# Optimization experiments

Measured on AMD Instinct MI355X. Metric: run time of the kernel, lower is better.

Reference implementation:

```python
import jax, jax.numpy as jnp
import numpy as np
from jax import lax

N = 100000      # nodes
E = 1600000     # edges
T = 8           # timesteps
DS, DT = 10, 20 # static / temporal features
GH = 64         # gnn_hidden
LH = 64         # lstm_hidden
EC = 64         # end_channels
OC = 1          # out_channels
EPS = 1e-5


def setup_inputs() -> dict:
    key = jax.random.key(0)
    ks = jax.random.split(key, 20)
    g = lambda i, shape, s=0.05: jax.random.normal(ks[i], shape, jnp.float32) * s
    return {
        "x": jax.random.normal(ks[0], (N, DS + DT, T), jnp.float32),
        "edge_index": jax.random.randint(ks[1], (2, E), 0, N, jnp.int64),
        # static encoder (computed in forward but unused downstream, kept for faithfulness)
        "W_static": g(2, (GH, DS)), "b_static": g(3, (GH,)),
        # LSTMCell: input_size = DT + GH, hidden = LH; gate order i,f,g,o
        "W_ih": g(4, (4 * LH, DT + GH)), "W_hh": g(5, (4 * LH, LH)),
        "b_ih": g(6, (4 * LH,)), "b_hh": g(7, (4 * LH,)),
        # GraphConv(lstm_hidden -> gnn_hidden): lin_rel (with bias) on aggregated msgs + lin_root (no bias)
        "W_rel": g(8, (GH, LH)), "b_rel": g(9, (GH,)), "W_root": g(10, (GH, LH)),
        # BatchNorm1d(GH+LH)
        "gamma": jnp.ones((GH + LH,), jnp.float32), "beta": jnp.zeros((GH + LH,), jnp.float32),
        # head: linear1(128->EC), linear2(EC->128), output_layer(128->OC)
        "W1": g(11, (EC, GH + LH)), "b1": g(12, (EC,)),
        "W2": g(13, (GH + LH, EC)), "b2": g(14, (GH + LH,)),
        "W_out": g(15, (OC, GH + LH)), "b_out": g(16, (OC,)),
    }


def reference(x, edge_index, W_static, b_static, W_ih, W_hh, b_ih, b_hh,
              W_rel, b_rel, W_root, gamma, beta, W1, b1, W2, b2, W_out, b_out):
    src, dst = edge_index[0], edge_index[1]
    x_static = x[:, :DS, 0]                      # [N, DS]
    x_temporal = x[:, DS:DS + DT, :]             # [N, DT, T]
    static_embed = x_static @ W_static.T + b_static  # computed but unused (matches source)

    xt_seq = jnp.transpose(x_temporal, (2, 0, 1))  # [T, N, DT]
    h0 = jnp.zeros((N, GH), jnp.float32)
    c0 = jnp.zeros((N, GH), jnp.float32)

    def step(carry, x_t):
        h, c = carry
        # GraphConv: sum-aggregate neighbor h, then linear (linear commutes with sum)
        agg = jax.ops.segment_sum(h[src], dst, num_segments=N)   # [N, LH]
        gnn_out = agg @ W_rel.T + b_rel + h @ W_root.T           # [N, GH]
        inp = jnp.concatenate([x_t, gnn_out], axis=1)            # [N, DT+GH]
        gates = inp @ W_ih.T + b_ih + h @ W_hh.T + b_hh          # [N, 4*LH]
        i, f, g_, o = jnp.split(gates, 4, axis=1)
        c_new = jax.nn.sigmoid(f) * c + jax.nn.sigmoid(i) * jnp.tanh(g_)
        h_new = jax.nn.sigmoid(o) * jnp.tanh(c_new)
        return (h_new, c_new), gnn_out

    (h, c), gnn_outs = lax.scan(step, (h0, c0), xt_seq)
    gnn_out = gnn_outs[-1]  # gnn output computed at the last timestep (pre-update h)

    fused = jnp.concatenate([h, gnn_out], axis=1)                # [N, GH+LH]
    # BatchNorm1d, training-mode batch statistics (dropout p set to 0)
    mean = fused.mean(axis=0)
    var = fused.var(axis=0)
    normed = (fused - mean) * lax.rsqrt(var + EPS) * gamma + beta
    h1 = jax.nn.relu(normed @ W1.T + b1)
    hidden = jax.nn.relu(h1 @ W2.T + b2)
    out = jax.nn.sigmoid(hidden @ W_out.T + b_out)               # binary task -> sigmoid
    return out
```

## Files before the change

kernel.cpp:

```cpp
#include <hip/hip_runtime.h>

#define NN 100000
#define NE 1600000
#define TT 8
#define KF 160
#define XSTR 24
#define HISTB 6250
#define NRANGE 8
#define RSPAN 12500

typedef __attribute__((ext_vector_type(8))) short bf16x8;
typedef __attribute__((ext_vector_type(4))) float f32x4;
typedef unsigned int uint_;
typedef unsigned short ushort_;
typedef __attribute__((ext_vector_type(4))) uint_ u32x4;

__device__ __forceinline__ float sigf(float x) { return 1.f / (1.f + __expf(-x)); }
__device__ __forceinline__ float tanhf_(float x) { return 1.f - 2.f / (__expf(2.f * x) + 1.f); }
__device__ __forceinline__ ushort_ f2b(float f) {
    uint_ u = __float_as_uint(f);
    u += 0x7fff + ((u >> 16) & 1);
    return (ushort_)(u >> 16);
}
__device__ __forceinline__ float bl(uint_ u) { return __uint_as_float(u << 16); }
__device__ __forceinline__ float bh(uint_ u) { return __uint_as_float(u & 0xffff0000u); }
__device__ __forceinline__ void acc8(float* a, uint4 v) {
    a[0] += bl(v.x); a[1] += bh(v.x); a[2] += bl(v.y); a[3] += bh(v.y);
    a[4] += bl(v.z); a[5] += bh(v.z); a[6] += bl(v.w); a[7] += bh(v.w);
}
__device__ __forceinline__ uint_ pk(float a, float b) {
    return (uint_)f2b(a) | ((uint_)f2b(b) << 16);
}
__device__ __forceinline__ uint4 ntld16(const void* p) {
    u32x4 v = __builtin_nontemporal_load((const u32x4*)p);
    return make_uint4(v[0], v[1], v[2], v[3]);
}

__global__ void k_detect(const int* __restrict__ ei, int* flag) {
    int i = blockIdx.x * 256 + threadIdx.x;
    if (ei[2 * i + 1] != 0) atomicOr(flag, 1);
}

__global__ void k_hist_xt(const int* __restrict__ ei, const int* __restrict__ flag, int* cnt,
                          const float* __restrict__ x, ushort_* __restrict__ xT) {
    int b = blockIdx.x;
    if (b < HISTB) {
        int e = b * 256 + threadIdx.x;
        if (e >= NE) return;
        int is32 = *flag;
        int d = is32 ? ei[NE + e] : ei[2 * (NE + e)];
        atomicAdd(&cnt[d], 1);
    } else {
        if (!xT) return;
        int i = (b - HISTB) * 256 + threadIdx.x;
        if (i >= NN * XSTR) return;
        int n = i / XSTR, kk = i - n * XSTR;
        if (kk < 20) {
            const float* xp = x + (size_t)n * 240 + (10 + kk) * 8;
#pragma unroll
            for (int t = 0; t < 8; t++) xT[(size_t)t * NN * XSTR + i] = f2b(xp[t]);
        } else {
#pragma unroll
            for (int t = 0; t < 8; t++) xT[(size_t)t * NN * XSTR + i] = 0;
        }
    }
}

__global__ void k_scanblk(const int* __restrict__ cnt, int* off, int* bsum) {
    __shared__ int tmp[1024];
    int i = blockIdx.x * 1024 + threadIdx.x;
    int v = (i < NN) ? cnt[i] : 0;
    tmp[threadIdx.x] = v;
    __syncthreads();
    for (int d = 1; d < 1024; d <<= 1) {
        int t = (threadIdx.x >= d) ? tmp[threadIdx.x - d] : 0;
        __syncthreads();
        tmp[threadIdx.x] += t;
        __syncthreads();
    }
    if (i < NN) off[i + 1] = tmp[threadIdx.x];
    if (threadIdx.x == 1023) bsum[blockIdx.x] = tmp[1023];
}

__global__ void k_scantop(int* bsum, int nb) {
    if (threadIdx.x == 0) {
        int run = 0;
        for (int b = 0; b < nb; b++) { int t = bsum[b]; bsum[b] = run; run += t; }
    }
}

__global__ void k_scanadd(int* off, const int* __restrict__ bsum) {
    int i = blockIdx.x * 1024 + threadIdx.x;
    if (i < NN) off[i + 1] += bsum[blockIdx.x];
    if (i == 0) off[0] = 0;
}

__global__ void k_scatter(const int* __restrict__ ei, const int* __restrict__ flag,
                          int* cursor, int* csr) {
    int b = blockIdx.x;
    int range = b & (NRANGE - 1), chunk = b >> 3;
    int e = chunk * 256 + threadIdx.x;
    if (e >= NE) return;
    int is32 = *flag;
    int d = is32 ? ei[NE + e] : ei[2 * (NE + e)];
    if (d / RSPAN != range) return;
    int s = is32 ? ei[e] : ei[2 * e];
    int pos = atomicAdd(&cursor[d], 1);
    csr[pos] = s;
}

__global__ void k_prep(const float* __restrict__ W_ih, const float* __restrict__ W_hh,
                       const float* __restrict__ b_ih, const float* __restrict__ b_hh,
                       const float* __restrict__ W_rel, const float* __restrict__ b_rel,
                       const float* __restrict__ W_root, ushort_* WgB, float* bgp) {
    int n = threadIdx.x;
    int k = blockIdx.x;
    if (k < KF) {
        float v = 0.f;
        if (n < 256) {
            int w = n >> 6, g = (n >> 4) & 3, j = w * 16 + (n & 15);
            int row = g * 64 + j;
            if (k < 20) {
                v = W_ih[row * 84 + k];
            } else if (k >= 24 && k < 88) {
                int kk = k - 24;
                float a = 0.f;
                for (int m = 0; m < 64; m++) a += W_ih[row * 84 + 20 + m] * W_rel[m * 64 + kk];
                v = a;
            } else if (k >= 88 && k < 152) {
                int kk = k - 88;
                float a = W_hh[row * 64 + kk];
                for (int m = 0; m < 64; m++) a += W_ih[row * 84 + 20 + m] * W_root[m * 64 + kk];
                v = a;
            }
        } else {
            int j = n - 256;
            if (k >= 24 && k < 88) v = W_rel[j * 64 + (k - 24)];
            else if (k >= 88 && k < 152) v = W_root[j * 64 + (k - 88)];
        }
        WgB[(size_t)n * KF + k] = f2b(v);
    } else {
        if (n < 256) {
            int j = n >> 2, g = n & 3;
            int row = g * 64 + j;
            float a = b_ih[row] + b_hh[row];
            for (int m = 0; m < 64; m++) a += W_ih[row * 84 + 20 + m] * b_rel[m];
            bgp[n] = a;
        } else {
            bgp[n] = b_rel[n - 256];
        }
    }
}

template <bool LAST>
__device__ __forceinline__ void step_body(const float* __restrict__ x,
                                          const ushort_* __restrict__ xT,
                                          const int* __restrict__ off,
                                          const int* __restrict__ csr,
                                          const ushort_* __restrict__ hbR,
                                          ushort_* __restrict__ hbW,
                                          float* __restrict__ hf,
                                          float* __restrict__ c,
                                          const ushort_* __restrict__ WgB,
                                          const float* __restrict__ bgp,
                                          float* __restrict__ gnn,
                                          float* __restrict__ sums,
                                          float* __restrict__ sumsq, int t) {
    __shared__ __align__(16) ushort_ Zs[64 * 168];
    const int tid = threadIdx.x;
    const int nblk = blockIdx.x * 64;
    const int w = tid >> 6, lane = tid & 63;
    const int q = lane >> 4, l16 = lane & 15;

#pragma unroll
    for (int i = 0; i < 3; ++i) {
        int slot = tid + 256 * i;
        int n = slot / 12, oo = slot - n * 12;
        int n_g = nblk + n;
        uint4 z = make_uint4(0, 0, 0, 0);
        if (n_g < NN) {
            if (oo < 3) {
                if (xT) {
                    z = ntld16(xT + ((size_t)t * NN + n_g) * XSTR + oo * 8);
                } else {
                    const float* xp = x + (size_t)n_g * 240 + 80 + (size_t)oo * 64 + t;
                    uint_ r[4];
#pragma unroll
                    for (int p = 0; p < 4; p++) {
                        int k0 = oo * 8 + p * 2;
                        ushort_ b0 = (k0 < 20) ? f2b(xp[p * 16]) : (ushort_)0;
                        ushort_ b1 = (k0 + 1 < 20) ? f2b(xp[p * 16 + 8]) : (ushort_)0;
                        r[p] = (uint_)b0 | ((uint_)b1 << 16);
                    }
                    z = make_uint4(r[0], r[1], r[2], r[3]);
                }
            } else if (oo < 11) {
                if (t > 0)
                    z = *(const uint4*)(hbR + (size_t)n_g * 64 + (oo - 3) * 8);
            }
        }
        int oct = (oo < 3) ? oo : ((oo < 11) ? (oo + 8) : 19);
        *(uint4*)(Zs + n * 168 + oct * 8) = z;
    }

    {
        int slot = tid >> 3;
        int l8 = tid & 7;
        for (int nn = slot; nn < 64; nn += 32) {
            int node = nblk + nn;
            float a[8];
#pragma unroll
            for (int i = 0; i < 8; i++) a[i] = 0.f;
            if (t > 0 && node < NN) {
                int e0 = off[node], e1 = off[node + 1];
                int e = e0;
                if (e + 8 <= e1) {
                    uint4 v[8];
#pragma unroll
                    for (int i = 0; i < 8; i++)
                        v[i] = *(const uint4*)(hbR + (size_t)csr[e + i] * 64 + l8 * 8);
                    e += 8;
                    for (; e + 8 <= e1; e += 8) {
#pragma unroll
                        for (int i = 0; i < 4; i++) {
                            acc8(a, v[i]);
                            v[i] = *(const uint4*)(hbR + (size_t)csr[e + i] * 64 + l8 * 8);
                        }
#pragma unroll
                        for (int i = 4; i < 8; i++) {
                            acc8(a, v[i]);
                            v[i] = *(const uint4*)(hbR + (size_t)csr[e + i] * 64 + l8 * 8);
                        }
                    }
#pragma unroll
                    for (int i = 0; i < 8; i++) acc8(a, v[i]);
                }
                for (; e < e1; e++) {
                    uint4 v0 = *(const uint4*)(hbR + (size_t)csr[e] * 64 + l8 * 8);
                    acc8(a, v0);
                }
            }
            uint4 o;
            o.x = pk(a[0], a[1]); o.y = pk(a[2], a[3]);
            o.z = pk(a[4], a[5]); o.w = pk(a[6], a[7]);
            *(uint4*)(Zs + nn * 168 + 24 + l8 * 8) = o;
        }
    }
    __syncthreads();

    const int j = w * 16 + l16;
    float sh = 0.f, sh2 = 0.f, sg = 0.f, sg2 = 0.f;

    if (LAST) {
        f32x4 accg[4];
#pragma unroll
        for (int mt = 0; mt < 4; mt++) accg[mt] = (f32x4)(0.f);
#pragma unroll
        for (int kt = 0; kt < 5; ++kt) {
            bf16x8 bfg = *(const bf16x8*)(WgB + (size_t)(256 + w * 16 + l16) * KF + kt * 32 + q * 8);
#pragma unroll
            for (int mt = 0; mt < 4; mt++) {
                bf16x8 af = *(const bf16x8*)(Zs + (mt * 16 + l16) * 168 + kt * 32 + q * 8);
                accg[mt] = __builtin_amdgcn_mfma_f32_16x16x32_bf16(af, bfg, accg[mt], 0, 0, 0);
            }
        }
        const float brl = bgp[256 + j];
#pragma unroll
        for (int mt = 0; mt < 4; ++mt)
#pragma unroll
            for (int r = 0; r < 4; ++r) {
                int node = nblk + mt * 16 + q * 4 + r;
                if (node < NN) {
                    float gn = accg[mt][r] + brl;
                    gnn[(size_t)node * 64 + j] = gn;
                    sg += gn; sg2 += gn * gn;
                }
            }
    }

    f32x4 acc[4][4];
#pragma unroll
    for (int mt = 0; mt < 4; mt++)
#pragma unroll
        for (int nt = 0; nt < 4; nt++) acc[mt][nt] = (f32x4)(0.f);

#pragma unroll
    for (int kt = 0; kt < 5; ++kt) {
        bf16x8 af[4], bf[4];
#pragma unroll
        for (int mt = 0; mt < 4; mt++)
            af[mt] = *(const bf16x8*)(Zs + (mt * 16 + l16) * 168 + kt * 32 + q * 8);
#pragma unroll
        for (int nt = 0; nt < 4; nt++) {
            int n = w * 64 + nt * 16 + l16;
            bf[nt] = *(const bf16x8*)(WgB + (size_t)n * KF + kt * 32 + q * 8);
        }
#pragma unroll
        for (int mt = 0; mt < 4; mt++)
#pragma unroll
            for (int nt = 0; nt < 4; nt++)
                acc[mt][nt] = __builtin_amdgcn_mfma_f32_16x16x32_bf16(af[mt], bf[nt], acc[mt][nt], 0, 0, 0);
    }

    const f32x4 bias = *(const f32x4*)(bgp + j * 4);

    __syncthreads();
    ushort_* Hs   = Zs;
    float*   CsLo = (float*)(Zs + 4096);

    float cnHi[8];
#pragma unroll
    for (int mt = 0; mt < 4; ++mt) {
#pragma unroll
        for (int r = 0; r < 4; ++r) {
            int nloc = mt * 16 + q * 4 + r;
            int node = nblk + nloc;
            float cn = 0.f, hn = 0.f;
            if (node < NN) {
                size_t idx = (size_t)node * 64 + j;
                float iv = sigf(acc[mt][0][r] + bias.x);
                float fv = sigf(acc[mt][1][r] + bias.y);
                float gv = tanhf_(acc[mt][2][r] + bias.z);
                float ov = sigf(acc[mt][3][r] + bias.w);
                float cold = 0.f;
                if (t > 0) cold = __builtin_nontemporal_load(c + idx);
                cn = fv * cold + iv * gv;
                hn = ov * tanhf_(cn);
                if (LAST) {
                    hf[idx] = hn;
                    sh += hn; sh2 += hn * hn;
                }
            }
            Hs[nloc * 64 + j] = f2b(hn);
            if (mt < 2) CsLo[nloc * 64 + j] = cn;
            else        cnHi[(mt - 2) * 4 + r] = cn;
        }
    }
    __syncthreads();
#pragma unroll
    for (int i = 0; i < 2; ++i) {
        int s = tid + 256 * i;
        {
            int n = s >> 3, part = s & 7;
            if (nblk + n < NN)
                *(uint4*)(hbW + (size_t)(nblk + n) * 64 + part * 8) =
                    *(const uint4*)(Hs + n * 64 + part * 8);
        }
        {
            int n = s >> 4, part = s & 15;
            if (nblk + n < NN)
                *(float4*)(c + (size_t)(nblk + n) * 64 + part * 4) =
                    *(const float4*)(CsLo + n * 64 + part * 4);
        }
    }
    __syncthreads();
    float* CsHi = (float*)Zs;
#pragma unroll
    for (int mt = 2; mt < 4; ++mt)
#pragma unroll
        for (int r = 0; r < 4; ++r) {
            int nloc = mt * 16 + q * 4 + r;
            CsHi[(nloc - 32) * 64 + j] = cnHi[(mt - 2) * 4 + r];
        }
    __syncthreads();
#pragma unroll
    for (int i = 0; i < 2; ++i) {
        int s = tid + 256 * i;
        int n = 32 + (s >> 4), part = s & 15;
        if (nblk + n < NN)
            *(float4*)(c + (size_t)(nblk + n) * 64 + part * 4) =
                *(const float4*)(CsHi + (n - 32) * 64 + part * 4);
    }

    if (LAST) {
#pragma unroll
        for (int d = 16; d < 64; d <<= 1) {
            sh += __shfl_xor(sh, d, 64);
            sh2 += __shfl_xor(sh2, d, 64);
            sg += __shfl_xor(sg, d, 64);
            sg2 += __shfl_xor(sg2, d, 64);
        }
        if (q == 0) {
            atomicAdd(&sums[j], sh);
            atomicAdd(&sumsq[j], sh2);
            atomicAdd(&sums[64 + j], sg);
            atomicAdd(&sumsq[64 + j], sg2);
        }
    }
}

__global__ __launch_bounds__(256, 4) void k_step(const float* __restrict__ x,
                                                 const ushort_* __restrict__ xT,
                                                 const int* __restrict__ off,
                                                 const int* __restrict__ csr,
                                                 const ushort_* __restrict__ hbR,
                                                 ushort_* __restrict__ hbW,
                                                 float* __restrict__ hf,
                                                 float* __restrict__ c,
                                                 const ushort_* __restrict__ WgB,
                                                 const float* __restrict__ bgp, int t) {
    step_body<false>(x, xT, off, csr, hbR, hbW, hf, c, WgB, bgp, nullptr, nullptr, nullptr, t);
}

__global__ __launch_bounds__(256, 4) void k_stepL(const float* __restrict__ x,
                                                  const ushort_* __restrict__ xT,
                                                  const int* __restrict__ off,
                                                  const int* __restrict__ csr,
                                                  const ushort_* __restrict__ hbR,
                                                  ushort_* __restrict__ hbW,
                                                  float* __restrict__ hf,
                                                  float* __restrict__ c,
                                                  const ushort_* __restrict__ WgB,
                                                  const float* __restrict__ bgp,
                                                  float* __restrict__ gnn,
                                                  float* __restrict__ sums,
                                                  float* __restrict__ sumsq, int t) {
    step_body<true>(x, xT, off, csr, hbR, hbW, hf, c, WgB, bgp, gnn, sums, sumsq, t);
}

__global__ __launch_bounds__(256) void k_head(const float* __restrict__ hf,
                                              const float* __restrict__ gnn,
                                              const float* __restrict__ sums,
                                              const float* __restrict__ sumsq,
                                              const float* __restrict__ gamma,
                                              const float* __restrict__ beta,
                                              const float* __restrict__ W1,
                                              const float* __restrict__ b1,
                                              const float* __restrict__ W2,
                                              const float* __restrict__ b2,
                                              const float* __restrict__ W_out,
                                              const float* __restrict__ b_out,
                                              float* __restrict__ out) {
    __shared__ __align__(16) ushort_ Zs[64 * 168];
    __shared__ __align__(16) ushort_ W1s[64 * 168];
    __shared__ __align__(16) ushort_ W2s[128 * 72];
    __shared__ __align__(16) ushort_ H1s[64 * 72];
    __shared__ float ab[256];
    __shared__ float Obuf[4][64];
    const int tid = threadIdx.x;
    const int w = tid >> 6, lane = tid & 63;
    const int q = lane >> 4, l16 = lane & 15;

    if (tid < 128) {
        float mean = sums[tid] / (float)NN;
        float var = sumsq[tid] / (float)NN - mean * mean;
        float a = gamma[tid] * rsqrtf(var + 1e-5f);
        ab[tid] = a;
        ab[128 + tid] = beta[tid] - mean * a;
    }
#pragma unroll
    for (int i = 0; i < 8; ++i) {
        int slot = tid + 256 * i;
        int jj = slot >> 5, k4 = slot & 31;
        float4 v = *(const float4*)(W1 + (size_t)jj * 128 + k4 * 4);
        *(uint2*)(W1s + jj * 168 + k4 * 4) = make_uint2(pk(v.x, v.y), pk(v.z, v.w));
    }
#pragma unroll
    for (int i = 0; i < 8; ++i) {
        int slot = tid + 256 * i;
        int jj = slot >> 4, k4 = slot & 15;
        float4 v = *(const float4*)(W2 + (size_t)jj * 64 + k4 * 4);
        *(uint2*)(W2s + jj * 72 + k4 * 4) = make_uint2(pk(v.x, v.y), pk(v.z, v.w));
    }
    const int j1 = w * 16 + l16;
    const float bb1 = b1[j1];
    const int j2a = (w * 2) * 16 + l16, j2b = (w * 2 + 1) * 16 + l16;
    const float bb2a = b2[j2a], bb2b = b2[j2b];
    const float woa = W_out[j2a], wob = W_out[j2b];
    const float bo = b_out[0];
    __syncthreads();

    const int NTILE = (NN + 63) / 64;
    for (int tile = blockIdx.x; tile < NTILE; tile += gridDim.x) {
        const int nblk = tile * 64;
#pragma unroll
        for (int i = 0; i < 8; ++i) {
            int slot = tid + 256 * i;
            int n = slot >> 5, f4 = slot & 31;
            int n_g = nblk + n;
            uint2 z = make_uint2(0, 0);
            if (n_g < NN) {
                const float* src = (f4 < 16) ? (hf + (size_t)n_g * 64 + f4 * 4)
                                             : (gnn + (size_t)n_g * 64 + (f4 - 16) * 4);
                float4 v = *(const float4*)src;
                int F = f4 * 4;
                z = make_uint2(pk(v.x * ab[F] + ab[128 + F], v.y * ab[F + 1] + ab[129 + F]),
                               pk(v.z * ab[F + 2] + ab[130 + F], v.w * ab[F + 3] + ab[131 + F]));
            }
            *(uint2*)(Zs + n * 168 + f4 * 4) = z;
        }
        __syncthreads();
        f32x4 acc1[4];
#pragma unroll
        for (int mt = 0; mt < 4; mt++) acc1[mt] = (f32x4)(0.f);
#pragma unroll
        for (int kt = 0; kt < 4; ++kt) {
            bf16x8 bfw = *(const bf16x8*)(W1s + j1 * 168 + kt * 32 + q * 8);
#pragma unroll
            for (int mt = 0; mt < 4; mt++) {
                bf16x8 af = *(const bf16x8*)(Zs + (mt * 16 + l16) * 168 + kt * 32 + q * 8);
                acc1[mt] = __builtin_amdgcn_mfma_f32_16x16x32_bf16(af, bfw, acc1[mt], 0, 0, 0);
            }
        }
#pragma unroll
        for (int mt = 0; mt < 4; mt++)
#pragma unroll
            for (int r = 0; r < 4; r++) {
                int nloc = mt * 16 + q * 4 + r;
                H1s[nloc * 72 + j1] = f2b(fmaxf(acc1[mt][r] + bb1, 0.f));
            }
        __syncthreads();
        f32x4 acc2[4][2];
#pragma unroll
        for (int mt = 0; mt < 4; mt++)
#pragma unroll
            for (int nt = 0; nt < 2; nt++) acc2[mt][nt] = (f32x4)(0.f);
#pragma unroll
        for (int kt = 0; kt < 2; ++kt) {
            bf16x8 bfa = *(const bf16x8*)(W2s + j2a * 72 + kt * 32 + q * 8);
            bf16x8 bfb = *(const bf16x8*)(W2s + j2b * 72 + kt * 32 + q * 8);
#pragma unroll
            for (int mt = 0; mt < 4; mt++) {
                bf16x8 af = *(const bf16x8*)(H1s + (mt * 16 + l16) * 72 + kt * 32 + q * 8);
                acc2[mt][0] = __builtin_amdgcn_mfma_f32_16x16x32_bf16(af, bfa, acc2[mt][0], 0, 0, 0);
                acc2[mt][1] = __builtin_amdgcn_mfma_f32_16x16x32_bf16(af, bfb, acc2[mt][1], 0, 0, 0);
            }
        }
#pragma unroll
        for (int mt = 0; mt < 4; mt++) {
#pragma unroll
            for (int r = 0; r < 4; r++) {
                float p = fmaxf(acc2[mt][0][r] + bb2a, 0.f) * woa +
                          fmaxf(acc2[mt][1][r] + bb2b, 0.f) * wob;
#pragma unroll
                for (int d = 1; d < 16; d <<= 1) p += __shfl_xor(p, d, 64);
                if (l16 == 0) Obuf[w][mt * 16 + q * 4 + r] = p;
            }
        }
        __syncthreads();
        if (tid < 64) {
            int n_g = nblk + tid;
            if (n_g < NN) {
                float s = Obuf[0][tid] + Obuf[1][tid] + Obuf[2][tid] + Obuf[3][tid];
                out[n_g] = sigf(s + bo);
            }
        }
        __syncthreads();
    }
}

extern "C" void kernel_launch(void* const* d_in, const int* in_sizes, int n_in,
                              void* d_out, int out_size, void* d_ws, size_t ws_size,
                              hipStream_t stream) {
    const float* x      = (const float*)d_in[0];
    const int*   ei     = (const int*)d_in[1];
    const float* W_ih   = (const float*)d_in[4];
    const float* W_hh   = (const float*)d_in[5];
    const float* b_ih   = (const float*)d_in[6];
    const float* b_hh   = (const float*)d_in[7];
    const float* W_rel  = (const float*)d_in[8];
    const float* b_rel  = (const float*)d_in[9];
    const float* W_root = (const float*)d_in[10];
    const float* gamma  = (const float*)d_in[11];
    const float* beta   = (const float*)d_in[12];
    const float* W1     = (const float*)d_in[13];
    const float* b1     = (const float*)d_in[14];
    const float* W2     = (const float*)d_in[15];
    const float* b2     = (const float*)d_in[16];
    const float* W_out  = (const float*)d_in[17];
    const float* b_out  = (const float*)d_in[18];
    float* out = (float*)d_out;

    char* ws = (char*)d_ws;
    size_t o = 0;
    auto carve = [&](size_t bytes) { char* p = ws + o; o += (bytes + 255) & ~(size_t)255; return p; };
    int*     off   = (int*)carve((NN + 1) * 4);
    int*     cnt   = (int*)carve(NN * 4);
    int*     bsum  = (int*)carve(128 * 4);
    int*     flag  = (int*)carve(256);
    int*     csr   = (int*)carve((size_t)NE * 4);
    float*   hf    = (float*)carve((size_t)NN * 64 * 4);
    float*   c     = (float*)carve((size_t)NN * 64 * 4);
    float*   gnn   = (float*)carve((size_t)NN * 64 * 4);
    ushort_* hbA   = (ushort_*)carve((size_t)NN * 64 * 2);
    ushort_* hbB   = (ushort_*)carve((size_t)NN * 64 * 2);
    ushort_* WgB   = (ushort_*)carve((size_t)320 * KF * 2);
    float*   bgp   = (float*)carve(320 * 4);
    float*   sums  = (float*)carve(128 * 4);
    float*   sumsq = (float*)carve(128 * 4);
    ushort_* xT = nullptr;
    size_t need_xt = (size_t)TT * NN * XSTR * 2;
    if (o + need_xt + 256 <= ws_size) xT = (ushort_*)carve(need_xt);

    const int nscan = (NN + 1023) / 1024;
    const int xtb = xT ? (NN * XSTR + 255) / 256 : 0;

    hipMemsetAsync(flag, 0, 4, stream);
    hipMemsetAsync(cnt, 0, NN * 4, stream);
    k_detect<<<16, 256, 0, stream>>>(ei, flag);
    k_hist_xt<<<HISTB + xtb, 256, 0, stream>>>(ei, flag, cnt, x, xT);
    k_scanblk<<<nscan, 1024, 0, stream>>>(cnt, off, bsum);
    k_scantop<<<1, 64, 0, stream>>>(bsum, nscan);
    k_scanadd<<<nscan, 1024, 0, stream>>>(off, bsum);
    hipMemcpyAsync(cnt, off, NN * 4, hipMemcpyDeviceToDevice, stream);
    k_scatter<<<(NE / 256) * NRANGE, 256, 0, stream>>>(ei, flag, cnt, csr);

    hipMemsetAsync(sums, 0, 1024, stream);
    k_prep<<<KF + 1, 320, 0, stream>>>(W_ih, W_hh, b_ih, b_hh, W_rel, b_rel, W_root, WgB, bgp);

    const int ngates = (NN + 63) / 64;
    for (int t = 0; t < TT; ++t) {
        ushort_* hbR = (t & 1) ? hbB : hbA;
        ushort_* hbW = (t & 1) ? hbA : hbB;
        if (t == TT - 1)
            k_stepL<<<ngates, 256, 0, stream>>>(x, xT, off, csr, hbR, hbW, hf, c,
                                                WgB, bgp, gnn, sums, sumsq, t);
        else
            k_step<<<ngates, 256, 0, stream>>>(x, xT, off, csr, hbR, hbW, hf, c,
                                               WgB, bgp, t);
    }

    k_head<<<512, 256, 0, stream>>>(hf, gnn, sums, sumsq, gamma, beta,
                                    W1, b1, W2, b2, W_out, b_out, out);
}
```

Before: 942.2 us.

## Balance neighbor gather by degree-sorted node pairing and stage cell state in LDS

Each block now ranks its 64 nodes by in-degree with a wavefront shuffle sort. The gather threads then pair the heaviest node with the lightest across two passes, to reduce load imbalance among the 8-lane groups during sum aggregation. Edge offsets are cached in shared memory. The previous cell state is prefetched into LDS with coalesced float4 loads instead of scattered per-element nontemporal loads in the gate epilogue. This adds 16KB+ of LDS per block, which may reduce occupancy, plus an extra barrier and the sort overhead.

After: 897.1 us. 1.05x faster.

```diff
diff --git a/kernel.cpp b/kernel.cpp
--- a/kernel.cpp
+++ b/kernel.cpp
@@ -167,10 +167,25 @@
                                           float* __restrict__ sums,
                                           float* __restrict__ sumsq, int t) {
     __shared__ __align__(16) ushort_ Zs[64 * 168];
+    __shared__ __align__(16) float Cs0[64 * 64];
+    __shared__ int sPerm[64];
+    __shared__ int sE0[64], sE1[64];
     const int tid = threadIdx.x;
     const int nblk = blockIdx.x * 64;
     const int w = tid >> 6, lane = tid & 63;
     const int q = lane >> 4, l16 = lane & 15;
+
+    if (tid < 64) {
+        int n_g = nblk + tid;
+        int e0 = (n_g < NN) ? off[n_g] : 0;
+        int e1 = (n_g < NN) ? off[n_g + 1] : 0;
+        sE0[tid] = e0; sE1[tid] = e1;
+        int key = ((e1 - e0) << 6) | tid;
+        int rank = 0;
+#pragma unroll
+        for (int m = 0; m < 64; m++) rank += (__shfl(key, m, 64) > key) ? 1 : 0;
+        sPerm[rank] = tid;
+    }
 
 #pragma unroll
     for (int i = 0; i < 3; ++i) {
@@ -202,17 +217,19 @@
         int oct = (oo < 3) ? oo : ((oo < 11) ? (oo + 8) : 19);
         *(uint4*)(Zs + n * 168 + oct * 8) = z;
     }
+    __syncthreads();
 
     {
         int slot = tid >> 3;
         int l8 = tid & 7;
-        for (int nn = slot; nn < 64; nn += 32) {
-            int node = nblk + nn;
+#pragma unroll
+        for (int pass = 0; pass < 2; ++pass) {
+            int nn = sPerm[pass ? (63 - slot) : slot];
             float a[8];
 #pragma unroll
             for (int i = 0; i < 8; i++) a[i] = 0.f;
-            if (t > 0 && node < NN) {
-                int e0 = off[node], e1 = off[node + 1];
+            if (t > 0) {
+                int e0 = sE0[nn], e1 = sE1[nn];
                 int e = e0;
                 if (e + 8 <= e1) {
                     uint4 v[8];
@@ -244,6 +261,18 @@
             o.x = pk(a[0], a[1]); o.y = pk(a[2], a[3]);
             o.z = pk(a[4], a[5]); o.w = pk(a[6], a[7]);
             *(uint4*)(Zs + nn * 168 + 24 + l8 * 8) = o;
+        }
+    }
+
+    if (t > 0) {
+        const float* cb = c + (size_t)nblk * 64;
+        const int lim = (NN - nblk) * 64;
+#pragma unroll
+        for (int k2 = 0; k2 < 4; ++k2) {
+            int f = (tid + 256 * k2) * 4;
+            float4 v = make_float4(0.f, 0.f, 0.f, 0.f);
+            if (f < lim) v = *(const float4*)(cb + f);
+            *(float4*)(Cs0 + f) = v;
         }
     }
     __syncthreads();
@@ -322,8 +351,7 @@
                 float fv = sigf(acc[mt][1][r] + bias.y);
                 float gv = tanhf_(acc[mt][2][r] + bias.z);
                 float ov = sigf(acc[mt][3][r] + bias.w);
-                float cold = 0.f;
-                if (t > 0) cold = __builtin_nontemporal_load(c + idx);
+                float cold = (t > 0) ? Cs0[nloc * 64 + j] : 0.f;
                 cn = fv * cold + iv * gv;
                 hn = ov * tanhf_(cn);
                 if (LAST) {
```
